# Performance work log

Measured on AMD Instinct MI355X. Metric: run time of the kernel, lower is better.

## Reference

```python
import jax, jax.numpy as jnp
import numpy as np

HIDDEN = 1024
HEADS = 16
HEAD_DIM = HIDDEN // HEADS
RANK = 256
B, S = 4, 2048


def setup_inputs() -> dict:
    key = jax.random.key(0)
    ks = jax.random.split(key, 10)
    sc_in = 1.0 / np.sqrt(HIDDEN)
    sc_r = 1.0 / np.sqrt(RANK)
    inp = {"hidden_states": jax.random.normal(ks[0], (B, S, HIDDEN), dtype=jnp.float32)}
    names = ["q", "k", "v"]
    for i, n in enumerate(names):
        inp[f"{n}A"] = jax.random.normal(ks[1 + 3 * i], (HIDDEN, RANK), dtype=jnp.float32) * sc_in
        inp[f"{n}B"] = jax.random.normal(ks[2 + 3 * i], (RANK, HIDDEN), dtype=jnp.float32) * sc_r
        inp[f"{n}b"] = jnp.zeros((HIDDEN,), dtype=jnp.float32)
    return inp


def _split_heads(x):
    # [B,S,H*D] -> [B,H,S,D]
    Bh, Sh, _ = x.shape
    return x.reshape(Bh, Sh, HEADS, HEAD_DIM).transpose(0, 2, 1, 3)


def reference(hidden_states, qA, qB, qb, kA, kB, kb, vA, vB, vb):
    # Low-rank projections: x @ A @ B + b (factorized linear)
    q = hidden_states @ qA @ qB + qb
    k = hidden_states @ kA @ kB + kb
    v = hidden_states @ vA @ vB + vb
    q = _split_heads(q)  # [B,H,S,D]
    k = _split_heads(k)
    v = _split_heads(v)
    scores = jnp.einsum("bhqd,bhkd->bhqk", q, k) / np.sqrt(HEAD_DIM)
    probs = jax.nn.softmax(scores, axis=-1)  # dropout is identity at inference
    ctx = jnp.einsum("bhqk,bhkd->bhqd", probs, v)
    ctx = ctx.transpose(0, 2, 1, 3).reshape(hidden_states.shape[0], hidden_states.shape[1], HIDDEN)
    return ctx
```

## Files before the change

kernel.cpp:

```cpp
#include <hip/hip_runtime.h>


typedef unsigned short u16;
typedef unsigned int   u32;
typedef __attribute__((ext_vector_type(4)))  float    f32x4;
typedef __attribute__((ext_vector_type(16))) float    f32x16;
typedef __attribute__((ext_vector_type(8)))  short    short8;
typedef __attribute__((ext_vector_type(8)))  _Float16 half8;
typedef __attribute__((ext_vector_type(4)))  u16      u16x4;

#define HID 1024
#define R_  256
#define S_  2048
#define B_  4
#define H_  16
#define D_  64
#define M_  (B_ * S_)

#define BM 128
#define BN 64
#define BK 64
#define LDP 72

#define KVB 64
#define SCL 0.18033688011112f
#define MSHIFT 8.0f

__device__ __forceinline__ u16 f2h(float f) {
    _Float16 h = (_Float16)f;
    return __builtin_bit_cast(u16, h);
}
__device__ __forceinline__ u32 pkrtz(float a, float b) {
    auto r = __builtin_amdgcn_cvt_pkrtz(a, b);
    return __builtin_bit_cast(u32, r);
}

__device__ __forceinline__ f32x4 mfma16(short8 a, short8 b, f32x4 c) {
    return __builtin_amdgcn_mfma_f32_16x16x32_f16(
        __builtin_bit_cast(half8, a), __builtin_bit_cast(half8, b), c, 0, 0, 0);
}
__device__ __forceinline__ f32x16 mfma32(short8 a, short8 b, f32x16 c) {
    return __builtin_amdgcn_mfma_f32_32x32x16_f16(
        __builtin_bit_cast(half8, a), __builtin_bit_cast(half8, b), c, 0, 0, 0);
}

#if defined(__has_builtin)
#if __has_builtin(__builtin_amdgcn_permlane32_swap)
#define HAVE_PLSWAP 1
#endif
#endif
__device__ __forceinline__ void plswap(u32 x, u32 y, u32& lo, u32& hi) {
#ifdef HAVE_PLSWAP
    typedef __attribute__((ext_vector_type(2))) unsigned uv2;
    uv2 r = __builtin_amdgcn_permlane32_swap(x, y, false, false);
    lo = r.x; hi = r.y;
#else
    u32 ty = (u32)__shfl_xor((int)y, 32);
    u32 tx = (u32)__shfl_xor((int)x, 32);
    int h = (threadIdx.x & 63) >> 5;
    lo = h ? ty : x;
    hi = h ? y : tx;
#endif
}

__global__ __launch_bounds__(256) void cvt_hs_kernel(const float* __restrict__ src,
                                                     u16* __restrict__ dst) {
    int i = (blockIdx.x * 256 + threadIdx.x) * 4;
    float4 v = *(const float4*)(src + i);
    u16x4 u;
    u[0] = f2h(v.x); u[1] = f2h(v.y); u[2] = f2h(v.z); u[3] = f2h(v.w);
    *(u16x4*)(dst + i) = u;
}

__global__ __launch_bounds__(256) void pack_weights_kernel(
    const float* __restrict__ qA, const float* __restrict__ kA, const float* __restrict__ vA,
    const float* __restrict__ qB, const float* __restrict__ kB, const float* __restrict__ vB,
    u16* __restrict__ At, u16* __restrict__ Bt) {
    int which = blockIdx.y;
    int o = blockIdx.x * 256 + threadIdx.x;
    if (which < 3) {
        const float* src = (which == 0) ? qA : (which == 1) ? kA : vA;
        u16* dst = At + (size_t)which * R_ * HID;
        int c = o >> 10, r = o & 1023;
        dst[o] = f2h(src[(size_t)r * R_ + c]);
    } else {
        int w = which - 3;
        const float* src = (w == 0) ? qB : (w == 1) ? kB : vB;
        float scl = (w == 0) ? SCL : 1.0f;
        u16* dst = Bt + (size_t)w * HID * R_;
        int c = o >> 8, r = o & 255;
        dst[o] = f2h(src[(size_t)r * HID + c] * scl);
    }
}

template <int KDIM, int NOUT, bool QKV_OUT>
__global__ __launch_bounds__(256, 2) void gemm_kernel(
    const u16* __restrict__ X, const u16* __restrict__ Wt, u16* __restrict__ Y,
    const float* __restrict__ bq, const float* __restrict__ bk, const float* __restrict__ bv) {
    const int w  = blockIdx.z;
    const int m0 = blockIdx.x * BM;
    const int n0 = blockIdx.y * BN;
    const u16* Xp = X + (QKV_OUT ? (size_t)w * M_ * KDIM : (size_t)0);
    const u16* Wp = Wt + (size_t)w * NOUT * KDIM;
    u16* Yp = Y + (size_t)w * M_ * NOUT;
    const float* bias = nullptr;
    float bscl = 1.0f;
    if constexpr (QKV_OUT) { bias = (w == 0) ? bq : (w == 1) ? bk : bv; bscl = (w == 0) ? SCL : 1.0f; }

    __shared__ __align__(16) u16 As[BM][LDP];
    __shared__ __align__(16) u16 Bs[BN][LDP];

    const int tid  = threadIdx.x;
    const int lane = tid & 63, wv = tid >> 6;
    const int l16 = lane & 15, lg = lane >> 4;
    const int wrow = (wv >> 1) * 64, wcol = (wv & 1) * 32;

    f32x4 acc[4][2];
#pragma unroll
    for (int i = 0; i < 4; ++i)
#pragma unroll
        for (int j = 0; j < 2; ++j) acc[i][j] = (f32x4){0.f, 0.f, 0.f, 0.f};

    for (int k0 = 0; k0 < KDIM; k0 += BK) {
#pragma unroll
        for (int p = 0; p < 4; ++p) {
            int r = p * 32 + (tid >> 3);
            int c8 = (tid & 7) * 8;
            *(short8*)&As[r][c8] = *(const short8*)(Xp + (size_t)(m0 + r) * KDIM + k0 + c8);
        }
#pragma unroll
        for (int p = 0; p < 2; ++p) {
            int r = p * 32 + (tid >> 3);
            int c8 = (tid & 7) * 8;
            *(short8*)&Bs[r][c8] = *(const short8*)(Wp + (size_t)(n0 + r) * KDIM + k0 + c8);
        }
        __syncthreads();
#pragma unroll
        for (int ks = 0; ks < 2; ++ks) {
            int kk = ks * 32 + 8 * lg;
            short8 af[4], bf[2];
#pragma unroll
            for (int ri = 0; ri < 4; ++ri) af[ri] = *(const short8*)&As[wrow + ri * 16 + l16][kk];
#pragma unroll
            for (int ci = 0; ci < 2; ++ci) bf[ci] = *(const short8*)&Bs[wcol + ci * 16 + l16][kk];
#pragma unroll
            for (int ri = 0; ri < 4; ++ri)
#pragma unroll
                for (int ci = 0; ci < 2; ++ci)
                    acc[ri][ci] = mfma16(af[ri], bf[ci], acc[ri][ci]);
        }
        __syncthreads();
    }
#pragma unroll
    for (int ri = 0; ri < 4; ++ri)
#pragma unroll
        for (int ci = 0; ci < 2; ++ci)
#pragma unroll
            for (int i = 0; i < 4; ++i) {
                int r = m0 + wrow + ri * 16 + lg * 4 + i;
                int c = n0 + wcol + ci * 16 + l16;
                float val = acc[ri][ci][i];
                if constexpr (QKV_OUT) val += bias[c] * bscl;
                Yp[(size_t)r * NOUT + c] = f2h(val);
            }
}

__global__ __launch_bounds__(256) void vtrans_kernel(const u16* __restrict__ v,
                                                     u16* __restrict__ vT) {
    int s0 = blockIdx.x * 64;
    int bh = blockIdx.y;
    int b = bh >> 4, h = bh & 15;
    __shared__ __align__(16) u16 tl[64][LDP];
    int t = threadIdx.x;
    int r = t >> 2;
#pragma unroll
    for (int i = 0; i < 2; ++i) {
        int c = i * 32 + (t & 3) * 8;
        *(short8*)&tl[r][c] = *(const short8*)(v + (size_t)(b * S_ + s0 + r) * HID + h * D_ + c);
    }
    __syncthreads();
    int d = t >> 2;
#pragma unroll
    for (int i = 0; i < 2; ++i) {
        int sb = i * 32 + (t & 3) * 8;
        short8 o;
#pragma unroll
        for (int j = 0; j < 8; ++j) o[j] = (short)tl[sb + j][d];
        *(short8*)(vT + ((size_t)bh * D_ + d) * S_ + s0 + sb) = o;
    }
}

__global__ __launch_bounds__(256) void attn_kernel(
    const u16* __restrict__ Q, const u16* __restrict__ K,
    const u16* __restrict__ VT, float* __restrict__ out) {
    const int bh = blockIdx.y, b = bh >> 4, h = bh & 15;
    const int tid = threadIdx.x, lane = tid & 63, wv = tid >> 6;
    const int l31 = lane & 31, hi = lane >> 5;
    const int q0 = blockIdx.x * 128 + wv * 32;
    const int rx = l31 & 7;

    __shared__ __align__(16) u16 Ks[2][KVB * 64];
    __shared__ __align__(16) u16 Vs[2][KVB * 64];

    short8 qf[4];
    {
        const u16* qp = Q + ((size_t)(b * S_ + q0 + l31)) * HID + h * D_ + 8 * hi;
#pragma unroll
        for (int ks = 0; ks < 4; ++ks) qf[ks] = *(const short8*)(qp + 16 * ks);
    }

    f32x16 ctx0, ctx1;
#pragma unroll
    for (int i = 0; i < 16; ++i) { ctx0[i] = 0.f; ctx1[i] = 0.f; }
    float la0 = 0.f, la1 = 0.f, la2 = 0.f, la3 = 0.f;

    const int r0p = tid >> 3, pos0 = tid & 7;
    const int rA = r0p, rB = r0p + 32;
    const int slA = pos0 ^ (rA & 7), slB = pos0 ^ (rB & 7);
    const size_t kofA = (size_t)rA * HID + slA * 8, kofB = (size_t)rB * HID + slB * 8;
    const size_t vofA = (size_t)rA * S_ + slA * 8,  vofB = (size_t)rB * S_ + slB * 8;
    const int wofA = rA * 64 + pos0 * 8, wofB = rB * 64 + pos0 * 8;

    const u16* Kcur = K + (size_t)(b * S_) * HID + h * D_;
    const u16* Vcur = VT + (size_t)bh * D_ * S_;

    short8 kst0, kst1, vst0, vst1;
    kst0 = *(const short8*)(Kcur + kofA);
    kst1 = *(const short8*)(Kcur + kofB);
    vst0 = *(const short8*)(Vcur + vofA);
    vst1 = *(const short8*)(Vcur + vofB);
    *(short8*)&Ks[0][wofA] = kst0;
    *(short8*)&Ks[0][wofB] = kst1;
    *(short8*)&Vs[0][wofA] = vst0;
    *(short8*)&Vs[0][wofB] = vst1;
    __syncthreads();

    for (int t = 0; t < S_ / KVB; ++t) {
        const int buf = t & 1;
        if (t + 1 < S_ / KVB) {
            const u16* Kn = Kcur + (size_t)(t + 1) * KVB * HID;
            const u16* Vn = Vcur + (size_t)(t + 1) * KVB;
            kst0 = *(const short8*)(Kn + kofA);
            kst1 = *(const short8*)(Kn + kofB);
            vst0 = *(const short8*)(Vn + vofA);
            vst1 = *(const short8*)(Vn + vofB);
        }

        f32x16 p0, p1;
#pragma unroll
        for (int i = 0; i < 16; ++i) { p0[i] = -MSHIFT; p1[i] = -MSHIFT; }
        const u16* kb = &Ks[buf][0];
#pragma unroll
        for (int ks = 0; ks < 4; ++ks) {
            int sl = (2 * ks + hi) ^ rx;
            short8 a0 = *(const short8*)(kb + l31 * 64 + sl * 8);
            short8 a1 = *(const short8*)(kb + (32 + l31) * 64 + sl * 8);
            p0 = mfma32(a0, qf[ks], p0);
            p1 = mfma32(a1, qf[ks], p1);
        }

#pragma unroll
        for (int i = 0; i < 16; ++i) {
            p0[i] = __builtin_amdgcn_exp2f(p0[i]);
            p1[i] = __builtin_amdgcn_exp2f(p1[i]);
        }
#pragma unroll
        for (int i = 0; i < 4; ++i) {
            la0 += p0[i] + p0[4 + i];
            la1 += p0[8 + i] + p0[12 + i];
            la2 += p1[i] + p1[4 + i];
            la3 += p1[8 + i] + p1[12 + i];
        }

        short8 pa[4];
#define PACK_CHUNK(pv, base, dst)                                   \
        {                                                           \
            u32 x0 = pkrtz(pv[base + 0], pv[base + 1]);             \
            u32 x1 = pkrtz(pv[base + 2], pv[base + 3]);             \
            u32 x2 = pkrtz(pv[base + 4], pv[base + 5]);             \
            u32 x3 = pkrtz(pv[base + 6], pv[base + 7]);             \
            u32 w0, w1, w2, w3;                                     \
            plswap(x0, x2, w0, w2);                                 \
            plswap(x1, x3, w1, w3);                                 \
            union { u32 w[4]; short8 v; } uu;                       \
            uu.w[0] = w0; uu.w[1] = w1; uu.w[2] = w2; uu.w[3] = w3; \
            dst = uu.v;                                             \
        }
        PACK_CHUNK(p0, 0, pa[0]);
        PACK_CHUNK(p0, 8, pa[1]);
        PACK_CHUNK(p1, 0, pa[2]);
        PACK_CHUNK(p1, 8, pa[3]);
#undef PACK_CHUNK

        const u16* vb = &Vs[buf][0];
#pragma unroll
        for (int c = 0; c < 4; ++c) {
            int sl = (2 * c + hi) ^ rx;
            short8 v0 = *(const short8*)(vb + l31 * 64 + sl * 8);
            short8 v1 = *(const short8*)(vb + (32 + l31) * 64 + sl * 8);
            ctx0 = mfma32(v0, pa[c], ctx0);
            ctx1 = mfma32(v1, pa[c], ctx1);
        }

        __syncthreads();
        if (t + 1 < S_ / KVB) {
            const int nb = 1 - buf;
            *(short8*)&Ks[nb][wofA] = kst0;
            *(short8*)&Ks[nb][wofB] = kst1;
            *(short8*)&Vs[nb][wofA] = vst0;
            *(short8*)&Vs[nb][wofB] = vst1;
        }
        __syncthreads();
    }

    float l = (la0 + la1) + (la2 + la3);
    l += __shfl_xor(l, 32);
    float invl = 1.0f / l;
    float* op = out + ((size_t)(b * S_ + q0 + l31)) * HID + h * D_;
#pragma unroll
    for (int g = 0; g < 4; ++g) {
        f32x4 o0, o1;
#pragma unroll
        for (int i = 0; i < 4; ++i) {
            o0[i] = ctx0[4 * g + i] * invl;
            o1[i] = ctx1[4 * g + i] * invl;
        }
        *(f32x4*)(op + 8 * g + 4 * hi) = o0;
        *(f32x4*)(op + 32 + 8 * g + 4 * hi) = o1;
    }
}

extern "C" void kernel_launch(void* const* d_in, const int* in_sizes, int n_in,
                              void* d_out, int out_size, void* d_ws, size_t ws_size,
                              hipStream_t stream) {
    const float* hs = (const float*)d_in[0];
    const float* qA = (const float*)d_in[1];
    const float* qB = (const float*)d_in[2];
    const float* qb = (const float*)d_in[3];
    const float* kA = (const float*)d_in[4];
    const float* kB = (const float*)d_in[5];
    const float* kb = (const float*)d_in[6];
    const float* vA = (const float*)d_in[7];
    const float* vB = (const float*)d_in[8];
    const float* vb = (const float*)d_in[9];

    char* ws = (char*)d_ws;
    size_t off = 0;
    u16* hsb = (u16*)(ws + off); off += (size_t)M_ * HID * 2;
    u16* At  = (u16*)(ws + off); off += (size_t)3 * R_ * HID * 2;
    u16* Bt  = (u16*)(ws + off); off += (size_t)3 * HID * R_ * 2;
    u16* T   = (u16*)(ws + off); off += (size_t)3 * M_ * R_ * 2;
    u16* QKV = (u16*)(ws + off); off += (size_t)3 * M_ * HID * 2;
    u16* VT  = (u16*)(ws + off);

    cvt_hs_kernel<<<dim3((M_ * HID) / 1024), 256, 0, stream>>>(hs, hsb);
    pack_weights_kernel<<<dim3(1024, 6), 256, 0, stream>>>(qA, kA, vA, qB, kB, vB, At, Bt);

    gemm_kernel<HID, R_, false><<<dim3(M_ / BM, R_ / BN, 3), 256, 0, stream>>>(
        hsb, At, T, nullptr, nullptr, nullptr);
    gemm_kernel<R_, HID, true><<<dim3(M_ / BM, HID / BN, 3), 256, 0, stream>>>(
        T, Bt, QKV, qb, kb, vb);

    vtrans_kernel<<<dim3(S_ / 64, B_ * H_), 256, 0, stream>>>(QKV + (size_t)2 * M_ * HID, VT);
    attn_kernel<<<dim3(S_ / 128, B_ * H_), 256, 0, stream>>>(
        QKV, QKV + (size_t)M_ * HID, VT, (float*)d_out);
}
```

Measured before the change: 178.5 us.

## Use direct global-to-LDS async loads with double buffering in GEMM and attention

Both the projection GEMM and the attention kernel now stage tiles with global_load_lds straight into swizzled, double-buffered shared memory. The next tile is prefetched while the current one is computed, and each iteration needs only one barrier. Register staging and the padded LDS layout are gone. The attention grid is remapped so each XCD handles a contiguous group of heads for better L2 locality. MFMA sections are wrapped in s_setprio, and the GEMM launch bound rises to 3 blocks per CU, which constrains registers and relies on barrier waits to complete the async loads.

```diff
diff --git a/kernel.cpp b/kernel.cpp
--- a/kernel.cpp
+++ b/kernel.cpp
@@ -42,6 +42,13 @@
 __device__ __forceinline__ f32x16 mfma32(short8 a, short8 b, f32x16 c) {
     return __builtin_amdgcn_mfma_f32_32x32x16_f16(
         __builtin_bit_cast(half8, a), __builtin_bit_cast(half8, b), c, 0, 0, 0);
+}
+
+__device__ __forceinline__ void gload16(const u16* g, u16* l) {
+    __builtin_amdgcn_global_load_lds(
+        (__attribute__((address_space(1))) const void*)g,
+        (__attribute__((address_space(3))) void*)l,
+        16, 0, 0);
 }
 
 #if defined(__has_builtin)
@@ -94,7 +101,7 @@
 }
 
 template <int KDIM, int NOUT, bool QKV_OUT>
-__global__ __launch_bounds__(256, 2) void gemm_kernel(
+__global__ __launch_bounds__(256, 3) void gemm_kernel(
     const u16* __restrict__ X, const u16* __restrict__ Wt, u16* __restrict__ Y,
     const float* __restrict__ bq, const float* __restrict__ bk, const float* __restrict__ bv) {
     const int w  = blockIdx.z;
@@ -107,50 +114,71 @@
     float bscl = 1.0f;
     if constexpr (QKV_OUT) { bias = (w == 0) ? bq : (w == 1) ? bk : bv; bscl = (w == 0) ? SCL : 1.0f; }
 
-    __shared__ __align__(16) u16 As[BM][LDP];
-    __shared__ __align__(16) u16 Bs[BN][LDP];
+    __shared__ __align__(16) u16 As[2][BM * BK];
+    __shared__ __align__(16) u16 Bs[2][BN * BK];
 
     const int tid  = threadIdx.x;
     const int lane = tid & 63, wv = tid >> 6;
     const int l16 = lane & 15, lg = lane >> 4;
     const int wrow = (wv >> 1) * 64, wcol = (wv & 1) * 32;
 
+    const int sr = lane >> 3, sp = lane & 7, sc = sp ^ sr;
+
+#define G_STAGE(bf, k0)                                                       \
+    {                                                                         \
+        _Pragma("unroll")                                                     \
+        for (int j = 0; j < 4; ++j) {                                         \
+            int ra = wv * 32 + j * 8;                                         \
+            gload16(Xp + (size_t)(m0 + ra + sr) * KDIM + (k0) + sc * 8,       \
+                    &As[bf][ra * 64]);                                        \
+        }                                                                     \
+        _Pragma("unroll")                                                     \
+        for (int j = 0; j < 2; ++j) {                                         \
+            int rb = wv * 16 + j * 8;                                         \
+            gload16(Wp + (size_t)(n0 + rb + sr) * KDIM + (k0) + sc * 8,       \
+                    &Bs[bf][rb * 64]);                                        \
+        }                                                                     \
+    }
+
     f32x4 acc[4][2];
 #pragma unroll
     for (int i = 0; i < 4; ++i)
 #pragma unroll
         for (int j = 0; j < 2; ++j) acc[i][j] = (f32x4){0.f, 0.f, 0.f, 0.f};
 
+    G_STAGE(0, 0);
+    int cur = 0;
     for (int k0 = 0; k0 < KDIM; k0 += BK) {
-#pragma unroll
-        for (int p = 0; p < 4; ++p) {
-            int r = p * 32 + (tid >> 3);
-            int c8 = (tid & 7) * 8;
-            *(short8*)&As[r][c8] = *(const short8*)(Xp + (size_t)(m0 + r) * KDIM + k0 + c8);
-        }
-#pragma unroll
-        for (int p = 0; p < 2; ++p) {
-            int r = p * 32 + (tid >> 3);
-            int c8 = (tid & 7) * 8;
-            *(short8*)&Bs[r][c8] = *(const short8*)(Wp + (size_t)(n0 + r) * KDIM + k0 + c8);
-        }
         __syncthreads();
+        if (k0 + BK < KDIM) G_STAGE(cur ^ 1, k0 + BK);
+        const u16* ab = &As[cur][0];
+        const u16* bb = &Bs[cur][0];
+        __builtin_amdgcn_s_setprio(1);
 #pragma unroll
         for (int ks = 0; ks < 2; ++ks) {
-            int kk = ks * 32 + 8 * lg;
             short8 af[4], bf[2];
 #pragma unroll
-            for (int ri = 0; ri < 4; ++ri) af[ri] = *(const short8*)&As[wrow + ri * 16 + l16][kk];
-#pragma unroll
-            for (int ci = 0; ci < 2; ++ci) bf[ci] = *(const short8*)&Bs[wcol + ci * 16 + l16][kk];
+            for (int ri = 0; ri < 4; ++ri) {
+                int r = wrow + ri * 16 + l16;
+                int c = ks * 4 + lg;
+                af[ri] = *(const short8*)(ab + r * 64 + ((c ^ (r & 7)) * 8));
+            }
+#pragma unroll
+            for (int ci = 0; ci < 2; ++ci) {
+                int r = wcol + ci * 16 + l16;
+                int c = ks * 4 + lg;
+                bf[ci] = *(const short8*)(bb + r * 64 + ((c ^ (r & 7)) * 8));
+            }
 #pragma unroll
             for (int ri = 0; ri < 4; ++ri)
 #pragma unroll
                 for (int ci = 0; ci < 2; ++ci)
                     acc[ri][ci] = mfma16(af[ri], bf[ci], acc[ri][ci]);
         }
-        __syncthreads();
-    }
+        __builtin_amdgcn_s_setprio(0);
+        cur ^= 1;
+    }
+#undef G_STAGE
 #pragma unroll
     for (int ri = 0; ri < 4; ++ri)
 #pragma unroll
@@ -193,10 +221,14 @@
 __global__ __launch_bounds__(256) void attn_kernel(
     const u16* __restrict__ Q, const u16* __restrict__ K,
     const u16* __restrict__ VT, float* __restrict__ out) {
-    const int bh = blockIdx.y, b = bh >> 4, h = bh & 15;
+    const int f = blockIdx.x;
+    const int xcd = f & 7, idx = f >> 3;
+    const int bh = xcd * 8 + (idx >> 4);
+    const int qt = idx & 15;
+    const int b = bh >> 4, h = bh & 15;
     const int tid = threadIdx.x, lane = tid & 63, wv = tid >> 6;
     const int l31 = lane & 31, hi = lane >> 5;
-    const int q0 = blockIdx.x * 128 + wv * 32;
+    const int q0 = qt * 128 + wv * 32;
     const int rx = l31 & 7;
 
     __shared__ __align__(16) u16 Ks[2][KVB * 64];
@@ -214,42 +246,33 @@
     for (int i = 0; i < 16; ++i) { ctx0[i] = 0.f; ctx1[i] = 0.f; }
     float la0 = 0.f, la1 = 0.f, la2 = 0.f, la3 = 0.f;
 
-    const int r0p = tid >> 3, pos0 = tid & 7;
-    const int rA = r0p, rB = r0p + 32;
-    const int slA = pos0 ^ (rA & 7), slB = pos0 ^ (rB & 7);
-    const size_t kofA = (size_t)rA * HID + slA * 8, kofB = (size_t)rB * HID + slB * 8;
-    const size_t vofA = (size_t)rA * S_ + slA * 8,  vofB = (size_t)rB * S_ + slB * 8;
-    const int wofA = rA * 64 + pos0 * 8, wofB = rB * 64 + pos0 * 8;
-
-    const u16* Kcur = K + (size_t)(b * S_) * HID + h * D_;
-    const u16* Vcur = VT + (size_t)bh * D_ * S_;
-
-    short8 kst0, kst1, vst0, vst1;
-    kst0 = *(const short8*)(Kcur + kofA);
-    kst1 = *(const short8*)(Kcur + kofB);
-    vst0 = *(const short8*)(Vcur + vofA);
-    vst1 = *(const short8*)(Vcur + vofB);
-    *(short8*)&Ks[0][wofA] = kst0;
-    *(short8*)&Ks[0][wofB] = kst1;
-    *(short8*)&Vs[0][wofA] = vst0;
-    *(short8*)&Vs[0][wofB] = vst1;
-    __syncthreads();
-
+    const u16* Kg = K + (size_t)(b * S_) * HID + h * D_;
+    const u16* Vg = VT + (size_t)bh * D_ * S_;
+    const int sr = lane >> 3, sp = lane & 7, sc = sp ^ sr;
+
+#define STAGE_ATTN(bf, kv0)                                                  \
+    {                                                                        \
+        _Pragma("unroll")                                                    \
+        for (int j = 0; j < 2; ++j) {                                        \
+            int rg = wv * 16 + j * 8;                                        \
+            gload16(Kg + (size_t)((kv0) + rg + sr) * HID + sc * 8,           \
+                    &Ks[bf][rg * 64]);                                       \
+            gload16(Vg + (size_t)(rg + sr) * S_ + (kv0) + sc * 8,            \
+                    &Vs[bf][rg * 64]);                                       \
+        }                                                                    \
+    }
+
+    STAGE_ATTN(0, 0);
+    int cur = 0;
     for (int t = 0; t < S_ / KVB; ++t) {
-        const int buf = t & 1;
-        if (t + 1 < S_ / KVB) {
-            const u16* Kn = Kcur + (size_t)(t + 1) * KVB * HID;
-            const u16* Vn = Vcur + (size_t)(t + 1) * KVB;
-            kst0 = *(const short8*)(Kn + kofA);
-            kst1 = *(const short8*)(Kn + kofB);
-            vst0 = *(const short8*)(Vn + vofA);
-            vst1 = *(const short8*)(Vn + vofB);
-        }
+        __syncthreads();
+        if (t + 1 < S_ / KVB) STAGE_ATTN(cur ^ 1, (t + 1) * KVB);
 
         f32x16 p0, p1;
 #pragma unroll
         for (int i = 0; i < 16; ++i) { p0[i] = -MSHIFT; p1[i] = -MSHIFT; }
-        const u16* kb = &Ks[buf][0];
+        const u16* kb = &Ks[cur][0];
+        __builtin_amdgcn_s_setprio(1);
 #pragma unroll
         for (int ks = 0; ks < 4; ++ks) {
             int sl = (2 * ks + hi) ^ rx;
@@ -258,6 +281,7 @@
             p0 = mfma32(a0, qf[ks], p0);
             p1 = mfma32(a1, qf[ks], p1);
         }
+        __builtin_amdgcn_s_setprio(0);
 
 #pragma unroll
         for (int i = 0; i < 16; ++i) {
@@ -292,7 +316,8 @@
         PACK_CHUNK(p1, 8, pa[3]);
 #undef PACK_CHUNK
 
-        const u16* vb = &Vs[buf][0];
+        const u16* vb = &Vs[cur][0];
+        __builtin_amdgcn_s_setprio(1);
 #pragma unroll
         for (int c = 0; c < 4; ++c) {
             int sl = (2 * c + hi) ^ rx;
@@ -301,17 +326,10 @@
             ctx0 = mfma32(v0, pa[c], ctx0);
             ctx1 = mfma32(v1, pa[c], ctx1);
         }
-
-        __syncthreads();
-        if (t + 1 < S_ / KVB) {
-            const int nb = 1 - buf;
-            *(short8*)&Ks[nb][wofA] = kst0;
-            *(short8*)&Ks[nb][wofB] = kst1;
-            *(short8*)&Vs[nb][wofA] = vst0;
-            *(short8*)&Vs[nb][wofB] = vst1;
-        }
-        __syncthreads();
-    }
+        __builtin_amdgcn_s_setprio(0);
+        cur ^= 1;
+    }
+#undef STAGE_ATTN
 
     float l = (la0 + la1) + (la2 + la3);
     l += __shfl_xor(l, 32);
@@ -362,6 +380,6 @@
         T, Bt, QKV, qb, kb, vb);
 
     vtrans_kernel<<<dim3(S_ / 64, B_ * H_), 256, 0, stream>>>(QKV + (size_t)2 * M_ * HID, VT);
-    attn_kernel<<<dim3(S_ / 128, B_ * H_), 256, 0, stream>>>(
+    attn_kernel<<<dim3(S_ / 8 / 16 * 64), 256, 0, stream>>>(
         QKV, QKV + (size_t)M_ * HID, VT, (float*)d_out);
 }
```

Measured after the change: 160.4 us. -10.1%, faster.
